# Kernel tuning notes

Measured on AMD Instinct MI355X. Metric: run time of the kernel, lower is better.

The kernel has to match this reference:

```python
import jax, jax.numpy as jnp
import numpy as np

VOCAB = 32000
HIDDEN = 2048
N_EXPERTS = 16
TOP_K = 2
EXPERT_VOCAB = VOCAB // N_EXPERTS  # 2000, divisible -> every expert slice fully valid
NUM_TOKENS = 4096


def setup_inputs() -> dict:
    key = jax.random.key(0)
    k1, k2, k3 = jax.random.split(key, 3)
    hidden_states = jax.random.normal(k1, (NUM_TOKENS, HIDDEN), dtype=jnp.float32)
    expert_weight = jax.random.normal(k2, (N_EXPERTS, EXPERT_VOCAB, HIDDEN), dtype=jnp.float32) * 0.02
    router_weight = jax.random.normal(k3, (N_EXPERTS, HIDDEN), dtype=jnp.float32) * 0.02
    return {"hidden_states": hidden_states, "expert_weight": expert_weight, "router_weight": router_weight}


def reference(hidden_states, expert_weight, router_weight):
    # Router: [T, E] scores -> softmax -> top_k expert ids per token
    router_logits = hidden_states @ router_weight.T
    routing_weights = jax.nn.softmax(router_logits, axis=-1)
    _, topk_ids = jax.lax.top_k(routing_weights, TOP_K)  # [T, K]

    # selection mask [T, E]: expert e selected for token t
    sel = jnp.any(topk_ids[:, :, None] == jnp.arange(N_EXPERTS)[None, None, :], axis=1)

    # Dense per-expert logits [T, E, EXPERT_VOCAB] (jit-friendly equivalent of
    # the gather-GEMM-scatter loop); unselected vocab slices get -inf.
    full = jnp.einsum('th,evh->tev', hidden_states, expert_weight)
    logits = jnp.where(sel[:, :, None], full, -jnp.inf)
    return logits.reshape(hidden_states.shape[0], VOCAB).astype(jnp.float32)
```

## Files before the change

### kernel.cpp

```cpp
#include <hip/hip_runtime.h>
#include <hip/hip_bf16.h>

#define NUM_TOKENS 4096
#define HIDDEN     2048
#define N_EXPERTS  16
#define TOP_K      2
#define EXPERT_VOCAB 2000
#define VOCAB      32000

#define NEG_FILL (-1.0e30f)

#define BM 128
#define BN 256
#define BK 32
#define LDA 40
#define THREADS 512

typedef float f32x4 __attribute__((ext_vector_type(4)));
typedef __bf16 bf16x8 __attribute__((ext_vector_type(8)));

__device__ __forceinline__ unsigned pack2(__bf16 a, __bf16 b) {
    unsigned short ua = __builtin_bit_cast(unsigned short, a);
    unsigned short ub = __builtin_bit_cast(unsigned short, b);
    return (unsigned)ua | ((unsigned)ub << 16);
}

__device__ __forceinline__ void cvt8h(f32x4 x, f32x4 y, uint4& hp) {
    __bf16 h[8];
    h[0] = (__bf16)x[0]; h[1] = (__bf16)x[1]; h[2] = (__bf16)x[2]; h[3] = (__bf16)x[3];
    h[4] = (__bf16)y[0]; h[5] = (__bf16)y[1]; h[6] = (__bf16)y[2]; h[7] = (__bf16)y[3];
    hp = (uint4){pack2(h[0],h[1]), pack2(h[2],h[3]), pack2(h[4],h[5]), pack2(h[6],h[7])};
}

__global__ void moe_router(const float* __restrict__ hs,
                           const float* __restrict__ rw,
                           int* __restrict__ counts,
                           int* __restrict__ lists,
                           unsigned* __restrict__ sel) {
    const int tid  = threadIdx.x;
    const int lane = tid & 63;
    const int t    = blockIdx.x * 4 + (tid >> 6);

    float acc[N_EXPERTS];
#pragma unroll
    for (int e = 0; e < N_EXPERTS; ++e) acc[e] = 0.f;

    const float* hrow = hs + (size_t)t * HIDDEN;
    for (int h = lane; h < HIDDEN; h += 64) {
        float x = hrow[h];
#pragma unroll
        for (int e = 0; e < N_EXPERTS; ++e)
            acc[e] += x * rw[e * HIDDEN + h];
    }
#pragma unroll
    for (int off = 32; off > 0; off >>= 1) {
#pragma unroll
        for (int e = 0; e < N_EXPERTS; ++e)
            acc[e] += __shfl_xor(acc[e], off);
    }
    int e1 = 0; float v1 = acc[0];
#pragma unroll
    for (int e = 1; e < N_EXPERTS; ++e)
        if (acc[e] > v1) { v1 = acc[e]; e1 = e; }
    int e2 = -1; float v2 = -__builtin_huge_valf();
#pragma unroll
    for (int e = 0; e < N_EXPERTS; ++e)
        if (e != e1 && acc[e] > v2) { v2 = acc[e]; e2 = e; }

    if (lane == 0) {
        sel[t] = (1u << e1) | (1u << e2);
        int p1 = atomicAdd(&counts[e1], 1); lists[e1 * NUM_TOKENS + p1] = t;
        int p2 = atomicAdd(&counts[e2], 1); lists[e2 * NUM_TOKENS + p2] = t;
    }
}

__global__ void moe_fill(const unsigned* __restrict__ sel, float* __restrict__ out) {
    const int t = blockIdx.x;
    const unsigned s = sel[t];
    f32x4* dst = (f32x4*)(out + (size_t)t * VOCAB);
    const f32x4 v = {NEG_FILL, NEG_FILL, NEG_FILL, NEG_FILL};
    for (int i = threadIdx.x; i < VOCAB / 4; i += 256) {
        int e = (i * 4) / EXPERT_VOCAB;
        if (!((s >> e) & 1u)) dst[i] = v;
    }
}

__global__ __launch_bounds__(THREADS)
void moe_gemm(const float* __restrict__ hs,
              const float* __restrict__ ew,
              const int* __restrict__ counts,
              const int* __restrict__ lists,
              float* __restrict__ out) {
    const int e  = blockIdx.z;
    const int ne = counts[e];
    const int row0 = blockIdx.y * BM;
    if (row0 >= ne) return;
    const int v0 = blockIdx.x * BN;

    __shared__ int toks[BM];
    __shared__ unsigned short Ah[BM * LDA];
    __shared__ unsigned short Bh[BN * LDA];

    const int tid = threadIdx.x;
    if (tid < BM) {
        int idx = row0 + tid;
        toks[tid] = (idx < ne) ? lists[e * NUM_TOKENS + idx] : -1;
    }
    __syncthreads();

    const int srow = tid >> 2;
    const int scq  = (tid & 3) * 8;
    const int stok = max(toks[srow], 0);
    const float* aptr = hs + (size_t)stok * HIDDEN + scq;
    const int br0 = min(v0 + srow,       EXPERT_VOCAB - 1);
    const int br1 = min(v0 + 128 + srow, EXPERT_VOCAB - 1);
    const float* bptr0 = ew + ((size_t)e * EXPERT_VOCAB + br0) * HIDDEN + scq;
    const float* bptr1 = ew + ((size_t)e * EXPERT_VOCAB + br1) * HIDDEN + scq;

    const int lane = tid & 63;
    const int w  = tid >> 6;
    const int wr = w & 1;
    const int wc = w >> 1;
    const int frow = lane & 15;
    const int k0l  = (lane >> 4) * 8;

    f32x4 acc[4][4];
#pragma unroll
    for (int m = 0; m < 4; ++m)
#pragma unroll
        for (int n = 0; n < 4; ++n)
            acc[m][n] = (f32x4){0.f, 0.f, 0.f, 0.f};

    f32x4 a0, a1, b00, b01, b10, b11;
    uint4 ahp, bhp0, bhp1;

    auto gload = [&](int k0) {
        a0  = *(const f32x4*)(aptr + k0);
        a1  = *(const f32x4*)(aptr + k0 + 4);
        b00 = *(const f32x4*)(bptr0 + k0);
        b01 = *(const f32x4*)(bptr0 + k0 + 4);
        b10 = *(const f32x4*)(bptr1 + k0);
        b11 = *(const f32x4*)(bptr1 + k0 + 4);
    };
    auto cvtall = [&]() {
        cvt8h(a0,  a1,  ahp);
        cvt8h(b00, b01, bhp0);
        cvt8h(b10, b11, bhp1);
    };

    gload(0);
    cvtall();

    const int NKT = HIDDEN / BK;
    for (int kt = 0; kt < NKT; ++kt) {
        *(uint4*)(Ah + srow * LDA + scq)         = ahp;
        *(uint4*)(Bh + srow * LDA + scq)         = bhp0;
        *(uint4*)(Bh + (128 + srow) * LDA + scq) = bhp1;
        __syncthreads();

        if (kt + 1 < NKT) gload((kt + 1) * BK);

        bf16x8 bh[4];
#pragma unroll
        for (int n = 0; n < 4; ++n) {
            int r = wc * 64 + n * 16 + frow;
            bh[n] = *(const bf16x8*)(Bh + r * LDA + k0l);
        }
#pragma unroll
        for (int m = 0; m < 4; ++m) {
            int r = wr * 64 + m * 16 + frow;
            bf16x8 ah = *(const bf16x8*)(Ah + r * LDA + k0l);
#pragma unroll
            for (int n = 0; n < 4; ++n)
                acc[m][n] = __builtin_amdgcn_mfma_f32_16x16x32_bf16(ah, bh[n], acc[m][n], 0, 0, 0);
        }

        if (kt + 1 < NKT) cvtall();
        __syncthreads();
    }

#pragma unroll
    for (int m = 0; m < 4; ++m) {
        int rbase = wr * 64 + m * 16 + (lane >> 4) * 4;
#pragma unroll
        for (int n = 0; n < 4; ++n) {
            int v = v0 + wc * 64 + n * 16 + (lane & 15);
            if (v < EXPERT_VOCAB) {
#pragma unroll
                for (int j = 0; j < 4; ++j) {
                    int tok = toks[rbase + j];
                    if (tok >= 0)
                        out[(size_t)tok * VOCAB + (size_t)e * EXPERT_VOCAB + v] = acc[m][n][j];
                }
            }
        }
    }
}

extern "C" void kernel_launch(void* const* d_in, const int* in_sizes, int n_in,
                              void* d_out, int out_size, void* d_ws, size_t ws_size,
                              hipStream_t stream) {
    const float* hs = (const float*)d_in[0];
    const float* ew = (const float*)d_in[1];
    const float* rw = (const float*)d_in[2];
    float* out = (float*)d_out;

    int* counts   = (int*)d_ws;
    int* lists    = counts + N_EXPERTS;
    unsigned* sel = (unsigned*)(lists + N_EXPERTS * NUM_TOKENS);

    hipMemsetAsync(counts, 0, N_EXPERTS * sizeof(int), stream);
    moe_router<<<NUM_TOKENS / 4, 256, 0, stream>>>(hs, rw, counts, lists, sel);
    moe_fill<<<NUM_TOKENS, 256, 0, stream>>>(sel, out);
    moe_gemm<<<dim3((EXPERT_VOCAB + BN - 1) / BN, NUM_TOKENS / BM, N_EXPERTS),
               THREADS, 0, stream>>>(hs, ew, counts, lists, out);
}
```

Before: 982.6 us.

## Pre-convert weights and activations to bf16, use direct global-to-LDS loads with swizzle

```diff
diff --git a/kernel.cpp b/kernel.cpp
--- a/kernel.cpp
+++ b/kernel.cpp
@@ -4,39 +4,61 @@
 #define NUM_TOKENS 4096
 #define HIDDEN     2048
 #define N_EXPERTS  16
-#define TOP_K      2
 #define EXPERT_VOCAB 2000
 #define VOCAB      32000
 
 #define NEG_FILL (-1.0e30f)
 
-#define BM 128
-#define BN 256
-#define BK 32
-#define LDA 40
-#define THREADS 512
-
 typedef float f32x4 __attribute__((ext_vector_type(4)));
 typedef __bf16 bf16x8 __attribute__((ext_vector_type(8)));
+typedef unsigned short ushort_t;
 
 __device__ __forceinline__ unsigned pack2(__bf16 a, __bf16 b) {
     unsigned short ua = __builtin_bit_cast(unsigned short, a);
     unsigned short ub = __builtin_bit_cast(unsigned short, b);
     return (unsigned)ua | ((unsigned)ub << 16);
 }
-
-__device__ __forceinline__ void cvt8h(f32x4 x, f32x4 y, uint4& hp) {
+__device__ __forceinline__ uint4 cvt8(f32x4 x, f32x4 y) {
     __bf16 h[8];
-    h[0] = (__bf16)x[0]; h[1] = (__bf16)x[1]; h[2] = (__bf16)x[2]; h[3] = (__bf16)x[3];
-    h[4] = (__bf16)y[0]; h[5] = (__bf16)y[1]; h[6] = (__bf16)y[2]; h[7] = (__bf16)y[3];
-    hp = (uint4){pack2(h[0],h[1]), pack2(h[2],h[3]), pack2(h[4],h[5]), pack2(h[6],h[7])};
-}
-
-__global__ void moe_router(const float* __restrict__ hs,
-                           const float* __restrict__ rw,
-                           int* __restrict__ counts,
-                           int* __restrict__ lists,
-                           unsigned* __restrict__ sel) {
+    h[0]=(__bf16)x[0]; h[1]=(__bf16)x[1]; h[2]=(__bf16)x[2]; h[3]=(__bf16)x[3];
+    h[4]=(__bf16)y[0]; h[5]=(__bf16)y[1]; h[6]=(__bf16)y[2]; h[7]=(__bf16)y[3];
+    return (uint4){pack2(h[0],h[1]), pack2(h[2],h[3]), pack2(h[4],h[5]), pack2(h[6],h[7])};
+}
+
+__device__ __forceinline__ void gload_lds16(const ushort_t* g, ushort_t* l) {
+    __builtin_amdgcn_global_load_lds(
+        (const __attribute__((address_space(1))) unsigned*)(const void*)g,
+        (__attribute__((address_space(3))) unsigned*)(void*)l, 16, 0, 0);
+}
+
+__global__ void moe_convert(const float* __restrict__ ew, const float* __restrict__ hs,
+                            ushort_t* __restrict__ ewb, ushort_t* __restrict__ hsb) {
+    const long long EWC = (long long)N_EXPERTS * EXPERT_VOCAB * (HIDDEN / 8);
+    const long long TOT = EWC + (long long)NUM_TOKENS * (HIDDEN / 8);
+    for (long long c = (long long)blockIdx.x * 256 + threadIdx.x; c < TOT;
+         c += (long long)gridDim.x * 256) {
+        if (c < EWC) {
+            int row = (int)(c >> 8);
+            int b   = (int)(c & 255);
+            int bs  = b ^ (row & 7);
+            const float* src = ew + (size_t)row * HIDDEN + bs * 8;
+            f32x4 x = *(const f32x4*)src, y = *(const f32x4*)(src + 4);
+            *(uint4*)(ewb + (size_t)row * HIDDEN + b * 8) = cvt8(x, y);
+        } else {
+            long long cc = c - EWC;
+            int row = (int)(cc >> 8), b = (int)(cc & 255);
+            const float* src = hs + (size_t)row * HIDDEN + b * 8;
+            f32x4 x = *(const f32x4*)src, y = *(const f32x4*)(src + 4);
+            *(uint4*)(hsb + (size_t)row * HIDDEN + b * 8) = cvt8(x, y);
+        }
+    }
+}
+
+__global__ void moe_router_fill(const float* __restrict__ hs,
+                                const float* __restrict__ rw,
+                                int* __restrict__ counts,
+                                int* __restrict__ lists,
+                                float* __restrict__ out) {
     const int tid  = threadIdx.x;
     const int lane = tid & 63;
     const int t    = blockIdx.x * 4 + (tid >> 6);
@@ -68,114 +90,112 @@
         if (e != e1 && acc[e] > v2) { v2 = acc[e]; e2 = e; }
 
     if (lane == 0) {
-        sel[t] = (1u << e1) | (1u << e2);
         int p1 = atomicAdd(&counts[e1], 1); lists[e1 * NUM_TOKENS + p1] = t;
         int p2 = atomicAdd(&counts[e2], 1); lists[e2 * NUM_TOKENS + p2] = t;
     }
-}
-
-__global__ void moe_fill(const unsigned* __restrict__ sel, float* __restrict__ out) {
-    const int t = blockIdx.x;
-    const unsigned s = sel[t];
+
+    const unsigned selmask = (1u << e1) | (1u << e2);
     f32x4* dst = (f32x4*)(out + (size_t)t * VOCAB);
-    const f32x4 v = {NEG_FILL, NEG_FILL, NEG_FILL, NEG_FILL};
-    for (int i = threadIdx.x; i < VOCAB / 4; i += 256) {
-        int e = (i * 4) / EXPERT_VOCAB;
-        if (!((s >> e) & 1u)) dst[i] = v;
-    }
-}
-
-__global__ __launch_bounds__(THREADS)
-void moe_gemm(const float* __restrict__ hs,
-              const float* __restrict__ ew,
-              const int* __restrict__ counts,
-              const int* __restrict__ lists,
+    const f32x4 nf = {NEG_FILL, NEG_FILL, NEG_FILL, NEG_FILL};
+    for (int i = lane; i < VOCAB / 4; i += 64) {
+        int e = i / 500;
+        if (!((selmask >> e) & 1u)) dst[i] = nf;
+    }
+}
+
+__global__ __launch_bounds__(512, 4)
+void moe_gemm(const ushort_t* __restrict__ hsb, const ushort_t* __restrict__ ewb,
+              const int* __restrict__ counts, const int* __restrict__ lists,
               float* __restrict__ out) {
-    const int e  = blockIdx.z;
+    const int bid  = blockIdx.x;
+    const int work = (bid & 7) * 512 + (bid >> 3);
+    const int e = work >> 8, x = (work >> 5) & 7, y = work & 31;
     const int ne = counts[e];
-    const int row0 = blockIdx.y * BM;
+    const int row0 = y * 128;
     if (row0 >= ne) return;
-    const int v0 = blockIdx.x * BN;
-
-    __shared__ int toks[BM];
-    __shared__ unsigned short Ah[BM * LDA];
-    __shared__ unsigned short Bh[BN * LDA];
-
-    const int tid = threadIdx.x;
-    if (tid < BM) {
-        int idx = row0 + tid;
-        toks[tid] = (idx < ne) ? lists[e * NUM_TOKENS + idx] : -1;
+    const int v0 = x * 256;
+
+    __shared__ int toks[128];
+    __shared__ ushort_t As[128 * 64];
+    __shared__ ushort_t Bs[256 * 64];
+
+    const int tid = threadIdx.x, lane = tid & 63, w = tid >> 6;
+    const int wr = w & 1, wc = w >> 1;
+
+    if (tid < 128) {
+        int i = row0 + tid;
+        toks[tid] = (i < ne) ? lists[e * NUM_TOKENS + i] : -1;
     }
     __syncthreads();
 
-    const int srow = tid >> 2;
-    const int scq  = (tid & 3) * 8;
-    const int stok = max(toks[srow], 0);
-    const float* aptr = hs + (size_t)stok * HIDDEN + scq;
-    const int br0 = min(v0 + srow,       EXPERT_VOCAB - 1);
-    const int br1 = min(v0 + 128 + srow, EXPERT_VOCAB - 1);
-    const float* bptr0 = ew + ((size_t)e * EXPERT_VOCAB + br0) * HIDDEN + scq;
-    const float* bptr1 = ew + ((size_t)e * EXPERT_VOCAB + br1) * HIDDEN + scq;
-
-    const int lane = tid & 63;
-    const int w  = tid >> 6;
-    const int wr = w & 1;
-    const int wc = w >> 1;
+    const int ar0 = tid >> 3,        ab0 = tid & 7;
+    const int ar1 = (tid + 512) >> 3, ab1 = tid & 7;
+    const ushort_t* ag0 = hsb + (size_t)max(toks[ar0], 0) * HIDDEN + ab0 * 8;
+    const ushort_t* ag1 = hsb + (size_t)max(toks[ar1], 0) * HIDDEN + ab1 * 8;
+    ushort_t* ad0 = As + (((ar0 * 128 + ab0 * 16) ^ ((ar0 & 7) << 4)) >> 1);
+    ushort_t* ad1 = As + (((ar1 * 128 + ab1 * 16) ^ ((ar1 & 7) << 4)) >> 1);
+
+    const ushort_t* bg[4];
+    ushort_t* blds[4];
+#pragma unroll
+    for (int q = 0; q < 4; ++q) {
+        int s = q * 512 + tid;
+        int r = s >> 3, b = s & 7;
+        int vr = min(v0 + r, EXPERT_VOCAB - 1);
+        bg[q]   = ewb + ((size_t)e * EXPERT_VOCAB + vr) * HIDDEN + b * 8;
+        blds[q] = Bs + (q * 512 + w * 64) * 8;
+    }
+
+    {
+        bf16x8 va = *(const bf16x8*)ag0;
+        bf16x8 vb = *(const bf16x8*)ag1;
+#pragma unroll
+        for (int q = 0; q < 4; ++q) gload_lds16(bg[q], blds[q]);
+        *(bf16x8*)ad0 = va;
+        *(bf16x8*)ad1 = vb;
+    }
+    __syncthreads();
+
+    f32x4 acc[4][4];
+#pragma unroll
+    for (int m = 0; m < 4; ++m)
+#pragma unroll
+        for (int n = 0; n < 4; ++n) acc[m][n] = (f32x4){0.f, 0.f, 0.f, 0.f};
+
     const int frow = lane & 15;
-    const int k0l  = (lane >> 4) * 8;
-
-    f32x4 acc[4][4];
-#pragma unroll
-    for (int m = 0; m < 4; ++m)
-#pragma unroll
-        for (int n = 0; n < 4; ++n)
-            acc[m][n] = (f32x4){0.f, 0.f, 0.f, 0.f};
-
-    f32x4 a0, a1, b00, b01, b10, b11;
-    uint4 ahp, bhp0, bhp1;
-
-    auto gload = [&](int k0) {
-        a0  = *(const f32x4*)(aptr + k0);
-        a1  = *(const f32x4*)(aptr + k0 + 4);
-        b00 = *(const f32x4*)(bptr0 + k0);
-        b01 = *(const f32x4*)(bptr0 + k0 + 4);
-        b10 = *(const f32x4*)(bptr1 + k0);
-        b11 = *(const f32x4*)(bptr1 + k0 + 4);
-    };
-    auto cvtall = [&]() {
-        cvt8h(a0,  a1,  ahp);
-        cvt8h(b00, b01, bhp0);
-        cvt8h(b10, b11, bhp1);
-    };
-
-    gload(0);
-    cvtall();
-
-    const int NKT = HIDDEN / BK;
+    const int kq   = lane >> 4;
+
+    const int NKT = HIDDEN / 64;
     for (int kt = 0; kt < NKT; ++kt) {
-        *(uint4*)(Ah + srow * LDA + scq)         = ahp;
-        *(uint4*)(Bh + srow * LDA + scq)         = bhp0;
-        *(uint4*)(Bh + (128 + srow) * LDA + scq) = bhp1;
+        bf16x8 na, nb;
+        if (kt + 1 < NKT) {
+            na = *(const bf16x8*)(ag0 + (kt + 1) * 64);
+            nb = *(const bf16x8*)(ag1 + (kt + 1) * 64);
+        }
+#pragma unroll
+        for (int kk = 0; kk < 2; ++kk) {
+            bf16x8 bfr[4];
+#pragma unroll
+            for (int n = 0; n < 4; ++n) {
+                int r = wc * 64 + n * 16 + frow;
+                bfr[n] = *(const bf16x8*)(Bs + (((r * 128 + kk * 64 + kq * 16) ^ ((r & 7) << 4)) >> 1));
+            }
+#pragma unroll
+            for (int m = 0; m < 4; ++m) {
+                int r = wr * 64 + m * 16 + frow;
+                bf16x8 afr = *(const bf16x8*)(As + (((r * 128 + kk * 64 + kq * 16) ^ ((r & 7) << 4)) >> 1));
+#pragma unroll
+                for (int n = 0; n < 4; ++n)
+                    acc[m][n] = __builtin_amdgcn_mfma_f32_16x16x32_bf16(afr, bfr[n], acc[m][n], 0, 0, 0);
+            }
+        }
         __syncthreads();
-
-        if (kt + 1 < NKT) gload((kt + 1) * BK);
-
-        bf16x8 bh[4];
-#pragma unroll
-        for (int n = 0; n < 4; ++n) {
-            int r = wc * 64 + n * 16 + frow;
-            bh[n] = *(const bf16x8*)(Bh + r * LDA + k0l);
-        }
-#pragma unroll
-        for (int m = 0; m < 4; ++m) {
-            int r = wr * 64 + m * 16 + frow;
-            bf16x8 ah = *(const bf16x8*)(Ah + r * LDA + k0l);
-#pragma unroll
-            for (int n = 0; n < 4; ++n)
-                acc[m][n] = __builtin_amdgcn_mfma_f32_16x16x32_bf16(ah, bh[n], acc[m][n], 0, 0, 0);
-        }
-
-        if (kt + 1 < NKT) cvtall();
+        if (kt + 1 < NKT) {
+#pragma unroll
+            for (int q = 0; q < 4; ++q) gload_lds16(bg[q] + (kt + 1) * 64, blds[q]);
+            *(bf16x8*)ad0 = na;
+            *(bf16x8*)ad1 = nb;
+        }
         __syncthreads();
     }
 
@@ -205,13 +225,14 @@
     const float* rw = (const float*)d_in[2];
     float* out = (float*)d_out;
 
-    int* counts   = (int*)d_ws;
-    int* lists    = counts + N_EXPERTS;
-    unsigned* sel = (unsigned*)(lists + N_EXPERTS * NUM_TOKENS);
-
-    hipMemsetAsync(counts, 0, N_EXPERTS * sizeof(int), stream);
-    moe_router<<<NUM_TOKENS / 4, 256, 0, stream>>>(hs, rw, counts, lists, sel);
-    moe_fill<<<NUM_TOKENS, 256, 0, stream>>>(sel, out);
-    moe_gemm<<<dim3((EXPERT_VOCAB + BN - 1) / BN, NUM_TOKENS / BM, N_EXPERTS),
-               THREADS, 0, stream>>>(hs, ew, counts, lists, out);
-}
+    char* ws = (char*)d_ws;
+    ushort_t* ewb = (ushort_t*)ws;
+    ushort_t* hsb = (ushort_t*)(ws + 131072000);
+    int* counts   = (int*)(ws + 131072000 + 16777216);
+    int* lists    = counts + 64;
+
+    hipMemsetAsync(counts, 0, 64 * sizeof(int), stream);
+    moe_convert<<<4096, 256, 0, stream>>>(ew, hs, ewb, hsb);
+    moe_router_fill<<<NUM_TOKENS / 4, 256, 0, stream>>>(hs, rw, counts, lists, out);
+    moe_gemm<<<N_EXPERTS * 8 * 32, 512, 0, stream>>>(hsb, ewb, counts, lists, out);
+}
```

Result: slower. 1.007 ms (+2.5%).
